# Kernel optimization log

Measured on AMD Instinct MI355X. Metric: run time of the kernel, lower is better.

The kernel has to match this reference:

```python
import jax, jax.numpy as jnp
import numpy as np

B, S, E, H = 4, 1024, 1024, 16
D = E // H  # per-head dim


def setup_inputs() -> dict:
    key = jax.random.key(0)
    ks = jax.random.split(key, 5)
    scale = 1.0 / np.sqrt(E)
    x = jax.random.normal(ks[0], (B, S, E), dtype=jnp.float32)
    Wq = jax.random.normal(ks[1], (H, E, D), dtype=jnp.float32) * scale
    Wk = jax.random.normal(ks[2], (H, E, D), dtype=jnp.float32) * scale
    Wv = jax.random.normal(ks[3], (H, E, D), dtype=jnp.float32) * scale
    W_O = jax.random.normal(ks[4], (E, E), dtype=jnp.float32) * scale
    return {"x": x, "Wq": Wq, "Wk": Wk, "Wv": Wv, "W_O": W_O}


def reference(x, Wq, Wk, Wv, W_O):
    # Batched-over-heads equivalent of the per-head Python loop.
    q = jnp.einsum('bse,hed->bhsd', x, Wq)
    k = jnp.einsum('bse,hed->bhsd', x, Wk)
    v = jnp.einsum('bse,hed->bhsd', x, Wv)
    scores = jnp.einsum('bhqd,bhkd->bhqk', q, k) / jnp.sqrt(jnp.float32(D))
    causal = jnp.tril(jnp.ones((S, S), dtype=bool))  # [S,S]
    scores = jnp.where(causal, scores, jnp.finfo(scores.dtype).min)
    attn = jax.nn.softmax(scores, axis=-1)
    heads = jnp.einsum('bhqk,bhkd->bhqd', attn, v)
    # concat heads along feature dim -> (B, S, E)
    concat = heads.transpose(0, 2, 1, 3).reshape(B, S, E)
    # Faithful to `self.W_O @ concatenated_outputs` (valid since S == E):
    # broadcasts W_O (E,E) against concat's trailing (S,E) matrices.
    output = jnp.matmul(W_O, concat)
    return output
```

## Files before the change

### kernel.cpp

```cpp
#include <hip/hip_runtime.h>
#include <hip/hip_bf16.h>
#include <math.h>

#define B_ 4
#define S_ 1024
#define E_ 1024
#define H_ 16
#define D_ 64

typedef __attribute__((ext_vector_type(8))) short   s16x8;
typedef __attribute__((ext_vector_type(8))) unsigned short u16x8;
typedef __attribute__((ext_vector_type(4))) unsigned short u16x4;
typedef __attribute__((ext_vector_type(4))) float   f32x4;
typedef unsigned short u16;

__device__ __forceinline__ u16 f2bf(float f) {
    union { float f; unsigned u; } v; v.f = f;
    unsigned u = v.u + 0x7FFFu + ((v.u >> 16) & 1u);
    return (u16)(u >> 16);
}
__device__ __forceinline__ float bf2f(u16 h) {
    union { unsigned u; float f; } v; v.u = ((unsigned)h) << 16;
    return v.f;
}
__device__ __forceinline__ void splitf(float f, u16& h, u16& l) {
    h = f2bf(f);
    l = f2bf(f - bf2f(h));
}

#define MFMA(a, b, c) __builtin_amdgcn_mfma_f32_16x16x32_bf16((a), (b), (c), 0, 0, 0)

#define LDR 40

__global__ __launch_bounds__(256) void split_f32(
    const float* __restrict__ src, u16* __restrict__ h, u16* __restrict__ l)
{
    const size_t i = ((size_t)blockIdx.x * 256 + threadIdx.x) * 8;
    f32x4 a = *(const f32x4*)(src + i);
    f32x4 b = *(const f32x4*)(src + i + 4);
    u16x8 hv, lv;
    #pragma unroll
    for (int j = 0; j < 4; j++) {
        u16 hh, ll;
        splitf(a[j], hh, ll); hv[j]     = hh; lv[j]     = ll;
        splitf(b[j], hh, ll); hv[j + 4] = hh; lv[j + 4] = ll;
    }
    *(u16x8*)(h + i) = hv;
    *(u16x8*)(l + i) = lv;
}

__global__ __launch_bounds__(256) void split_wT(
    const float* __restrict__ Wq, const float* __restrict__ Wk, const float* __restrict__ Wv,
    u16* __restrict__ wth, u16* __restrict__ wtl)
{
    __shared__ float T[64][65];
    const int e0 = blockIdx.x * 64;
    const int h  = blockIdx.y;
    const int w  = blockIdx.z;
    const float* W = (w == 0) ? Wq : (w == 1) ? Wk : Wv;

    const int tid = threadIdx.x;
    const int r4  = tid >> 4;
    const int c4  = (tid & 15) * 4;

    #pragma unroll
    for (int p = 0; p < 4; p++) {
        const int r = p * 16 + r4;
        f32x4 v = *(const f32x4*)(W + ((size_t)h * E_ + e0 + r) * D_ + c4);
        #pragma unroll
        for (int j = 0; j < 4; j++) T[r][c4 + j] = v[j];
    }
    __syncthreads();
    #pragma unroll
    for (int p = 0; p < 4; p++) {
        const int d = p * 16 + r4;
        u16x4 oh, ol;
        #pragma unroll
        for (int j = 0; j < 4; j++) {
            u16 hh, ll;
            splitf(T[c4 + j][d], hh, ll);
            oh[j] = hh; ol[j] = ll;
        }
        const size_t n   = (size_t)w * 1024 + h * 64 + d;
        const size_t off = n * E_ + e0 + c4;
        *(u16x4*)(wth + off) = oh;
        *(u16x4*)(wtl + off) = ol;
    }
}

__global__ __launch_bounds__(256) void qkv_gemm(
    const u16* __restrict__ xh, const u16* __restrict__ xl,
    const u16* __restrict__ wth, const u16* __restrict__ wtl,
    u16* __restrict__ qh, u16* __restrict__ ql,
    u16* __restrict__ kh, u16* __restrict__ kl,
    u16* __restrict__ vth, u16* __restrict__ vtl)
{
    __shared__ __align__(16) u16 Ah[128][LDR], Al[128][LDR], Bh[128][LDR], Bl[128][LDR];

    const int tid = threadIdx.x;
    const int m0  = blockIdx.x * 128;
    const int n0  = blockIdx.y * 128;
    const int w   = n0 >> 10;

    const int wid  = tid >> 6, lane = tid & 63;
    const int wr   = wid >> 1, wc = wid & 1;
    const int lrow = lane & 15, lk = lane >> 4;

    const int sr = tid >> 1;
    const int sh = (tid & 1) * 16;

    f32x4 acc[4][4] = {};

    for (int k0 = 0; k0 < E_; k0 += 32) {
        __syncthreads();
        {
            const size_t ao = (size_t)(m0 + sr) * E_ + k0 + sh;
            *(u16x8*)&Ah[sr][sh]     = *(const u16x8*)(xh + ao);
            *(u16x8*)&Ah[sr][sh + 8] = *(const u16x8*)(xh + ao + 8);
            *(u16x8*)&Al[sr][sh]     = *(const u16x8*)(xl + ao);
            *(u16x8*)&Al[sr][sh + 8] = *(const u16x8*)(xl + ao + 8);
            const size_t bo = (size_t)(n0 + sr) * E_ + k0 + sh;
            *(u16x8*)&Bh[sr][sh]     = *(const u16x8*)(wth + bo);
            *(u16x8*)&Bh[sr][sh + 8] = *(const u16x8*)(wth + bo + 8);
            *(u16x8*)&Bl[sr][sh]     = *(const u16x8*)(wtl + bo);
            *(u16x8*)&Bl[sr][sh + 8] = *(const u16x8*)(wtl + bo + 8);
        }
        __syncthreads();

        s16x8 fXh[4], fXl[4], fWh[4], fWl[4];
        #pragma unroll
        for (int i = 0; i < 4; i++) {
            fXh[i] = *(const s16x8*)&Ah[wr * 64 + i * 16 + lrow][lk * 8];
            fXl[i] = *(const s16x8*)&Al[wr * 64 + i * 16 + lrow][lk * 8];
            fWh[i] = *(const s16x8*)&Bh[wc * 64 + i * 16 + lrow][lk * 8];
            fWl[i] = *(const s16x8*)&Bl[wc * 64 + i * 16 + lrow][lk * 8];
        }
        __builtin_amdgcn_s_setprio(1);
        if (w < 2) {
            #pragma unroll
            for (int i = 0; i < 4; i++)
                #pragma unroll
                for (int j = 0; j < 4; j++) {
                    acc[i][j] = MFMA(fWh[i], fXh[j], acc[i][j]);
                    acc[i][j] = MFMA(fWl[i], fXh[j], acc[i][j]);
                    acc[i][j] = MFMA(fWh[i], fXl[j], acc[i][j]);
                }
        } else {
            #pragma unroll
            for (int i = 0; i < 4; i++)
                #pragma unroll
                for (int j = 0; j < 4; j++) {
                    acc[i][j] = MFMA(fXh[i], fWh[j], acc[i][j]);
                    acc[i][j] = MFMA(fXl[i], fWh[j], acc[i][j]);
                    acc[i][j] = MFMA(fXh[i], fWl[j], acc[i][j]);
                }
        }
        __builtin_amdgcn_s_setprio(0);
    }

    const int nloc = n0 & 1023;
    if (w < 2) {
        u16* Yh = (w == 0) ? qh : kh;
        u16* Yl = (w == 0) ? ql : kl;
        const float sc = (w == 0) ? 0.125f : 1.0f;
        #pragma unroll
        for (int i = 0; i < 4; i++) {
            const int nn = nloc + wc * 64 + i * 16 + lk * 4;
            const int hh2 = nn >> 6, d0 = nn & 63;
            #pragma unroll
            for (int j = 0; j < 4; j++) {
                const int mrow = m0 + wr * 64 + j * 16 + lrow;
                const int b = mrow >> 10, s = mrow & 1023;
                u16x4 oh, ol;
                #pragma unroll
                for (int r = 0; r < 4; r++) {
                    u16 hhv, llv;
                    splitf(acc[i][j][r] * sc, hhv, llv);
                    oh[r] = hhv; ol[r] = llv;
                }
                const size_t off = (((size_t)b * H_ + hh2) * S_ + s) * D_ + d0;
                *(u16x4*)(Yh + off) = oh;
                *(u16x4*)(Yl + off) = ol;
            }
        }
    } else {
        #pragma unroll
        for (int i = 0; i < 4; i++) {
            const int mrow = m0 + wr * 64 + i * 16 + lk * 4;
            const int b = mrow >> 10, s = mrow & 1023;
            #pragma unroll
            for (int j = 0; j < 4; j++) {
                const int nn = nloc + wc * 64 + j * 16 + lrow;
                const int hh2 = nn >> 6, d0 = nn & 63;
                u16x4 oh, ol;
                #pragma unroll
                for (int r = 0; r < 4; r++) {
                    u16 hhv, llv;
                    splitf(acc[i][j][r], hhv, llv);
                    oh[r] = hhv; ol[r] = llv;
                }
                const size_t off = (((size_t)b * H_ + hh2) * D_ + d0) * S_ + s;
                *(u16x4*)(vth + off) = oh;
                *(u16x4*)(vtl + off) = ol;
            }
        }
    }
}

__global__ __launch_bounds__(256) void attn(
    const u16* __restrict__ qh, const u16* __restrict__ ql,
    const u16* __restrict__ kh, const u16* __restrict__ kl,
    const u16* __restrict__ vth, const u16* __restrict__ vtl,
    u16* __restrict__ CTh, u16* __restrict__ CTl)
{
    const int qt = 15 - blockIdx.x;
    const int bh = blockIdx.y;

    __shared__ __align__(16) u16 Kh[64][72], Kl[64][72];
    __shared__ __align__(16) u16 Vh[64][72], Vl[64][72];
    __shared__ __align__(16) u16 Ph[4][16][72], Pl[4][16][72];

    const int tid = threadIdx.x, wid = tid >> 6, lane = tid & 63;
    const int lrow = lane & 15, lk = lane >> 4;
    const int q0g = qt * 64 + wid * 16;

    s16x8 fQh[2], fQl[2];
    {
        const size_t qoff = ((size_t)bh * S_ + q0g + lrow) * D_;
        #pragma unroll
        for (int ks = 0; ks < 2; ks++) {
            fQh[ks] = *(const s16x8*)(qh + qoff + ks * 32 + lk * 8);
            fQl[ks] = *(const s16x8*)(ql + qoff + ks * 32 + lk * 8);
        }
    }

    f32x4 accO[4] = {};
    float m_r[4], l_r[4];
    #pragma unroll
    for (int r = 0; r < 4; r++) { m_r[r] = -INFINITY; l_r[r] = 0.0f; }

    const u16* Kbh = kh  + (size_t)bh * S_ * D_;
    const u16* Kbl = kl  + (size_t)bh * S_ * D_;
    const u16* Vbh = vth + (size_t)bh * D_ * S_;
    const u16* Vbl = vtl + (size_t)bh * D_ * S_;

    const int rk = tid >> 2, ck = (tid & 3) * 16;

    u16x8 pf0, pf1, pf2, pf3, pf4, pf5, pf6, pf7;
#define ISSUE(c0_) { \
        const size_t ko = (size_t)((c0_) + rk) * D_ + ck; \
        pf0 = *(const u16x8*)(Kbh + ko);     pf1 = *(const u16x8*)(Kbh + ko + 8); \
        pf2 = *(const u16x8*)(Kbl + ko);     pf3 = *(const u16x8*)(Kbl + ko + 8); \
        const size_t vo = (size_t)rk * S_ + (c0_) + ck; \
        pf4 = *(const u16x8*)(Vbh + vo);     pf5 = *(const u16x8*)(Vbh + vo + 8); \
        pf6 = *(const u16x8*)(Vbl + vo);     pf7 = *(const u16x8*)(Vbl + vo + 8); }

    ISSUE(0)

    for (int t = 0; t <= qt; t++) {
        const int c0 = t * 64;
        __syncthreads();
        *(u16x8*)&Kh[rk][ck]     = pf0;  *(u16x8*)&Kh[rk][ck + 8] = pf1;
        *(u16x8*)&Kl[rk][ck]     = pf2;  *(u16x8*)&Kl[rk][ck + 8] = pf3;
        *(u16x8*)&Vh[rk][ck]     = pf4;  *(u16x8*)&Vh[rk][ck + 8] = pf5;
        *(u16x8*)&Vl[rk][ck]     = pf6;  *(u16x8*)&Vl[rk][ck + 8] = pf7;
        __syncthreads();

        if (t < qt) ISSUE(c0 + 64)

        f32x4 accS[4] = {};
        __builtin_amdgcn_s_setprio(1);
        #pragma unroll
        for (int nf = 0; nf < 4; nf++) {
            #pragma unroll
            for (int ks = 0; ks < 2; ks++) {
                const s16x8 kfh = *(const s16x8*)&Kh[nf * 16 + lrow][ks * 32 + lk * 8];
                const s16x8 kfl = *(const s16x8*)&Kl[nf * 16 + lrow][ks * 32 + lk * 8];
                accS[nf] = MFMA(fQh[ks], kfh, accS[nf]);
                accS[nf] = MFMA(fQl[ks], kfh, accS[nf]);
                accS[nf] = MFMA(fQh[ks], kfl, accS[nf]);
            }
        }
        __builtin_amdgcn_s_setprio(0);

        if (c0 + 63 > q0g) {
            #pragma unroll
            for (int nf = 0; nf < 4; nf++)
                #pragma unroll
                for (int r = 0; r < 4; r++) {
                    if (c0 + nf * 16 + lrow > q0g + lk * 4 + r) accS[nf][r] = -INFINITY;
                }
        }

        float rs[4];
        #pragma unroll
        for (int r = 0; r < 4; r++) {
            float v = fmaxf(fmaxf(accS[0][r], accS[1][r]), fmaxf(accS[2][r], accS[3][r]));
            #pragma unroll
            for (int d_ = 1; d_ < 16; d_ <<= 1) v = fmaxf(v, __shfl_xor(v, d_));
            const float mnew = fmaxf(m_r[r], v);
            rs[r] = __expf(m_r[r] - mnew);
            m_r[r] = mnew;
            float sum = 0.0f;
            #pragma unroll
            for (int nf = 0; nf < 4; nf++) {
                const float p = __expf(accS[nf][r] - mnew);
                accS[nf][r] = p;
                sum += p;
            }
            #pragma unroll
            for (int d_ = 1; d_ < 16; d_ <<= 1) sum += __shfl_xor(sum, d_);
            l_r[r] = l_r[r] * rs[r] + sum;
        }

        #pragma unroll
        for (int nf = 0; nf < 4; nf++)
            #pragma unroll
            for (int r = 0; r < 4; r++) {
                u16 hh, ll;
                splitf(accS[nf][r], hh, ll);
                Ph[wid][lk * 4 + r][nf * 16 + lrow] = hh;
                Pl[wid][lk * 4 + r][nf * 16 + lrow] = ll;
            }
        #pragma unroll
        for (int df = 0; df < 4; df++)
            #pragma unroll
            for (int r = 0; r < 4; r++) accO[df][r] *= rs[r];

        s16x8 fPh[2], fPl[2];
        #pragma unroll
        for (int ks = 0; ks < 2; ks++) {
            fPh[ks] = *(const s16x8*)&Ph[wid][lrow][ks * 32 + lk * 8];
            fPl[ks] = *(const s16x8*)&Pl[wid][lrow][ks * 32 + lk * 8];
        }
        __builtin_amdgcn_s_setprio(1);
        #pragma unroll
        for (int df = 0; df < 4; df++) {
            #pragma unroll
            for (int ks = 0; ks < 2; ks++) {
                const s16x8 vfh = *(const s16x8*)&Vh[df * 16 + lrow][ks * 32 + lk * 8];
                const s16x8 vfl = *(const s16x8*)&Vl[df * 16 + lrow][ks * 32 + lk * 8];
                accO[df] = MFMA(fPh[ks], vfh, accO[df]);
                accO[df] = MFMA(fPl[ks], vfh, accO[df]);
                accO[df] = MFMA(fPh[ks], vfl, accO[df]);
            }
        }
        __builtin_amdgcn_s_setprio(0);
    }
#undef ISSUE

    const int b = bh >> 4, h = bh & 15;
    float inv[4];
    #pragma unroll
    for (int r = 0; r < 4; r++) inv[r] = 1.0f / l_r[r];
    #pragma unroll
    for (int df = 0; df < 4; df++) {
        const int e = h * 64 + df * 16 + lrow;
        const int s = q0g + lk * 4;
        u16x4 oh, ol;
        #pragma unroll
        for (int r = 0; r < 4; r++) {
            u16 hh, ll;
            splitf(accO[df][r] * inv[r], hh, ll);
            oh[r] = hh; ol[r] = ll;
        }
        const size_t off = ((size_t)b * E_ + e) * S_ + s;
        *(u16x4*)(CTh + off) = oh;
        *(u16x4*)(CTl + off) = ol;
    }
}

__global__ __launch_bounds__(256) void out_gemm(
    const u16* __restrict__ CTh, const u16* __restrict__ CTl,
    const u16* __restrict__ woh, const u16* __restrict__ wol,
    float* __restrict__ out)
{
    __shared__ __align__(16) u16 Ah[128][LDR], Al[128][LDR], Bh[128][LDR], Bl[128][LDR];

    const int tid = threadIdx.x;
    const int j0 = blockIdx.x * 128;
    const int i0 = blockIdx.y * 128;
    const int b  = blockIdx.z;

    const int wid = tid >> 6, lane = tid & 63;
    const int wr = wid >> 1, wc = wid & 1;
    const int lrow = lane & 15, lk = lane >> 4;

    const int sr = tid >> 1;
    const int sh = (tid & 1) * 16;

    f32x4 acc[4][4] = {};

    for (int k0 = 0; k0 < S_; k0 += 32) {
        __syncthreads();
        {
            const size_t ao = ((size_t)b * E_ + j0 + sr) * S_ + k0 + sh;
            *(u16x8*)&Ah[sr][sh]     = *(const u16x8*)(CTh + ao);
            *(u16x8*)&Ah[sr][sh + 8] = *(const u16x8*)(CTh + ao + 8);
            *(u16x8*)&Al[sr][sh]     = *(const u16x8*)(CTl + ao);
            *(u16x8*)&Al[sr][sh + 8] = *(const u16x8*)(CTl + ao + 8);
            const size_t bo = (size_t)(i0 + sr) * S_ + k0 + sh;
            *(u16x8*)&Bh[sr][sh]     = *(const u16x8*)(woh + bo);
            *(u16x8*)&Bh[sr][sh + 8] = *(const u16x8*)(woh + bo + 8);
            *(u16x8*)&Bl[sr][sh]     = *(const u16x8*)(wol + bo);
            *(u16x8*)&Bl[sr][sh + 8] = *(const u16x8*)(wol + bo + 8);
        }
        __syncthreads();

        s16x8 fAh[4], fAl[4], fBh[4], fBl[4];
        #pragma unroll
        for (int i = 0; i < 4; i++) {
            fAh[i] = *(const s16x8*)&Ah[wr * 64 + i * 16 + lrow][lk * 8];
            fAl[i] = *(const s16x8*)&Al[wr * 64 + i * 16 + lrow][lk * 8];
            fBh[i] = *(const s16x8*)&Bh[wc * 64 + i * 16 + lrow][lk * 8];
            fBl[i] = *(const s16x8*)&Bl[wc * 64 + i * 16 + lrow][lk * 8];
        }
        __builtin_amdgcn_s_setprio(1);
        #pragma unroll
        for (int i = 0; i < 4; i++)
            #pragma unroll
            for (int j = 0; j < 4; j++) {
                acc[i][j] = MFMA(fAh[i], fBh[j], acc[i][j]);
                acc[i][j] = MFMA(fAl[i], fBh[j], acc[i][j]);
                acc[i][j] = MFMA(fAh[i], fBl[j], acc[i][j]);
            }
        __builtin_amdgcn_s_setprio(0);
    }

    #pragma unroll
    for (int i = 0; i < 4; i++) {
        const int jj = j0 + wr * 64 + i * 16 + lk * 4;
        #pragma unroll
        for (int j = 0; j < 4; j++) {
            const int ii = i0 + wc * 64 + j * 16 + lrow;
            float* dst = out + ((size_t)b * E_ + ii) * E_ + jj;
            *(f32x4*)dst = acc[i][j];
        }
    }
}

extern "C" void kernel_launch(void* const* d_in, const int* in_sizes, int n_in,
                              void* d_out, int out_size, void* d_ws, size_t ws_size,
                              hipStream_t stream)
{
    const float* x   = (const float*)d_in[0];
    const float* Wq  = (const float*)d_in[1];
    const float* Wk  = (const float*)d_in[2];
    const float* Wv  = (const float*)d_in[3];
    const float* W_O = (const float*)d_in[4];
    float* out = (float*)d_out;

    const size_t N = (size_t)B_ * S_ * E_;
    u16* p = (u16*)d_ws;
    u16* qh  = p;            u16* ql  = p + 1 * N;
    u16* kh  = p + 2 * N;    u16* kl  = p + 3 * N;
    u16* vth = p + 4 * N;    u16* vtl = p + 5 * N;
    u16* xh  = p + 6 * N;    u16* xl  = p + 7 * N;
    u16* wth = p + 8 * N;
    u16* wtl = wth + (size_t)3 * E_ * E_;
    u16* CTh = xh;           u16* CTl = xl;
    u16* woh = wth;          u16* wol = wtl;

    split_f32<<<2048, 256, 0, stream>>>(x, xh, xl);
    split_wT<<<dim3(16, 16, 3), 256, 0, stream>>>(Wq, Wk, Wv, wth, wtl);
    qkv_gemm<<<dim3(32, 24), 256, 0, stream>>>(xh, xl, wth, wtl, qh, ql, kh, kl, vth, vtl);
    split_f32<<<512, 256, 0, stream>>>(W_O, woh, wol);
    attn<<<dim3(16, 64), 256, 0, stream>>>(qh, ql, kh, kl, vth, vtl, CTh, CTl);
    out_gemm<<<dim3(8, 8, 4), 256, 0, stream>>>(CTh, CTl, woh, wol, out);
}
```

Measured before the change: 349.0 us.

## Pre-tile GEMM operands into contiguous 128x32 blocks and load via global_load_lds

The split kernels now write x, the QKV weights, W_O and the attention output in a block-tiled layout where each 128x32 K-slice is contiguous. The QKV and output GEMMs can then fill LDS with direct global-to-LDS 16-byte loads, one wave per operand, instead of loading into registers and storing to LDS. LDS rows lose their padding (stride 32 instead of 40), so fragment reads may hit bank conflicts. W_O's low half now sits at a different workspace offset.

```diff
diff --git a/kernel.cpp b/kernel.cpp
--- a/kernel.cpp
+++ b/kernel.cpp
@@ -30,12 +30,20 @@
 
 #define MFMA(a, b, c) __builtin_amdgcn_mfma_f32_16x16x32_bf16((a), (b), (c), 0, 0, 0)
 
-#define LDR 40
-
-__global__ __launch_bounds__(256) void split_f32(
-    const float* __restrict__ src, u16* __restrict__ h, u16* __restrict__ l)
+__device__ __forceinline__ void gload16(const u16* g, u16* l) {
+    __builtin_amdgcn_global_load_lds(
+        (const __attribute__((address_space(1))) void*)g,
+        (__attribute__((address_space(3))) void*)l, 16, 0, 0);
+}
+
+#define TILE_E   4096
+#define BLK_E    131072
+
+__global__ __launch_bounds__(256) void tile_rows(
+    const float* __restrict__ src, u16* __restrict__ th, u16* __restrict__ tl)
 {
     const size_t i = ((size_t)blockIdx.x * 256 + threadIdx.x) * 8;
+    const int m = (int)(i >> 10), e = (int)(i & 1023);
     f32x4 a = *(const f32x4*)(src + i);
     f32x4 b = *(const f32x4*)(src + i + 4);
     u16x8 hv, lv;
@@ -45,11 +53,13 @@
         splitf(a[j], hh, ll); hv[j]     = hh; lv[j]     = ll;
         splitf(b[j], hh, ll); hv[j + 4] = hh; lv[j + 4] = ll;
     }
-    *(u16x8*)(h + i) = hv;
-    *(u16x8*)(l + i) = lv;
-}
-
-__global__ __launch_bounds__(256) void split_wT(
+    const int mblk = m >> 7, row = m & 127, ks = e >> 5, col = e & 31;
+    const size_t off = ((size_t)(mblk * 32 + ks) * 128 + row) * 32 + col;
+    *(u16x8*)(th + off) = hv;
+    *(u16x8*)(tl + off) = lv;
+}
+
+__global__ __launch_bounds__(256) void tile_w(
     const float* __restrict__ Wq, const float* __restrict__ Wk, const float* __restrict__ Wv,
     u16* __restrict__ wth, u16* __restrict__ wtl)
 {
@@ -71,6 +81,9 @@
         for (int j = 0; j < 4; j++) T[r][c4 + j] = v[j];
     }
     __syncthreads();
+    const int nblk = w * 8 + (h >> 1);
+    const int ks   = (e0 + c4) >> 5;
+    const int col  = (e0 + c4) & 31;
     #pragma unroll
     for (int p = 0; p < 4; p++) {
         const int d = p * 16 + r4;
@@ -81,49 +94,49 @@
             splitf(T[c4 + j][d], hh, ll);
             oh[j] = hh; ol[j] = ll;
         }
-        const size_t n   = (size_t)w * 1024 + h * 64 + d;
-        const size_t off = n * E_ + e0 + c4;
+        const int row = (h & 1) * 64 + d;
+        const size_t off = ((size_t)(nblk * 32 + ks) * 128 + row) * 32 + col;
         *(u16x4*)(wth + off) = oh;
         *(u16x4*)(wtl + off) = ol;
     }
 }
 
 __global__ __launch_bounds__(256) void qkv_gemm(
-    const u16* __restrict__ xh, const u16* __restrict__ xl,
+    const u16* __restrict__ xsh, const u16* __restrict__ xsl,
     const u16* __restrict__ wth, const u16* __restrict__ wtl,
     u16* __restrict__ qh, u16* __restrict__ ql,
     u16* __restrict__ kh, u16* __restrict__ kl,
     u16* __restrict__ vth, u16* __restrict__ vtl)
 {
-    __shared__ __align__(16) u16 Ah[128][LDR], Al[128][LDR], Bh[128][LDR], Bl[128][LDR];
-
-    const int tid = threadIdx.x;
-    const int m0  = blockIdx.x * 128;
-    const int n0  = blockIdx.y * 128;
-    const int w   = n0 >> 10;
+    __shared__ __align__(16) u16 Ah[128][32], Al[128][32], Bh[128][32], Bl[128][32];
+
+    const int tid  = threadIdx.x;
+    const int mblk = blockIdx.x;
+    const int nblk = blockIdx.y;
+    const int n0   = nblk * 128;
+    const int w    = n0 >> 10;
 
     const int wid  = tid >> 6, lane = tid & 63;
     const int wr   = wid >> 1, wc = wid & 1;
     const int lrow = lane & 15, lk = lane >> 4;
 
-    const int sr = tid >> 1;
-    const int sh = (tid & 1) * 16;
+    const u16* gsrc;
+    u16* lbase;
+    if      (wid == 0) { gsrc = xsh + (size_t)mblk * BLK_E; lbase = &Ah[0][0]; }
+    else if (wid == 1) { gsrc = xsl + (size_t)mblk * BLK_E; lbase = &Al[0][0]; }
+    else if (wid == 2) { gsrc = wth + (size_t)nblk * BLK_E; lbase = &Bh[0][0]; }
+    else               { gsrc = wtl + (size_t)nblk * BLK_E; lbase = &Bl[0][0]; }
 
     f32x4 acc[4][4] = {};
 
-    for (int k0 = 0; k0 < E_; k0 += 32) {
+    for (int ks = 0; ks < 32; ks++) {
         __syncthreads();
         {
-            const size_t ao = (size_t)(m0 + sr) * E_ + k0 + sh;
-            *(u16x8*)&Ah[sr][sh]     = *(const u16x8*)(xh + ao);
-            *(u16x8*)&Ah[sr][sh + 8] = *(const u16x8*)(xh + ao + 8);
-            *(u16x8*)&Al[sr][sh]     = *(const u16x8*)(xl + ao);
-            *(u16x8*)&Al[sr][sh + 8] = *(const u16x8*)(xl + ao + 8);
-            const size_t bo = (size_t)(n0 + sr) * E_ + k0 + sh;
-            *(u16x8*)&Bh[sr][sh]     = *(const u16x8*)(wth + bo);
-            *(u16x8*)&Bh[sr][sh + 8] = *(const u16x8*)(wth + bo + 8);
-            *(u16x8*)&Bl[sr][sh]     = *(const u16x8*)(wtl + bo);
-            *(u16x8*)&Bl[sr][sh + 8] = *(const u16x8*)(wtl + bo + 8);
+            const u16* s = gsrc + (size_t)ks * TILE_E + lane * 8;
+            u16* l = lbase + lane * 8;
+            #pragma unroll
+            for (int c = 0; c < 8; c++)
+                gload16(s + c * 512, l + c * 512);
         }
         __syncthreads();
 
@@ -158,6 +171,7 @@
         __builtin_amdgcn_s_setprio(0);
     }
 
+    const int m0   = mblk * 128;
     const int nloc = n0 & 1023;
     if (w < 2) {
         u16* Yh = (w == 0) ? qh : kh;
@@ -353,10 +367,12 @@
     float inv[4];
     #pragma unroll
     for (int r = 0; r < 4; r++) inv[r] = 1.0f / l_r[r];
+    const int s0 = q0g + lk * 4;
+    const int kst = s0 >> 5, col = s0 & 31;
     #pragma unroll
     for (int df = 0; df < 4; df++) {
         const int e = h * 64 + df * 16 + lrow;
-        const int s = q0g + lk * 4;
+        const int jblk = e >> 7, row = e & 127;
         u16x4 oh, ol;
         #pragma unroll
         for (int r = 0; r < 4; r++) {
@@ -364,7 +380,8 @@
             splitf(accO[df][r] * inv[r], hh, ll);
             oh[r] = hh; ol[r] = ll;
         }
-        const size_t off = ((size_t)b * E_ + e) * S_ + s;
+        const size_t off = (size_t)b * 1048576 +
+                           ((size_t)(jblk * 32 + kst) * 128 + row) * 32 + col;
         *(u16x4*)(CTh + off) = oh;
         *(u16x4*)(CTl + off) = ol;
     }
@@ -375,35 +392,34 @@
     const u16* __restrict__ woh, const u16* __restrict__ wol,
     float* __restrict__ out)
 {
-    __shared__ __align__(16) u16 Ah[128][LDR], Al[128][LDR], Bh[128][LDR], Bl[128][LDR];
-
-    const int tid = threadIdx.x;
-    const int j0 = blockIdx.x * 128;
-    const int i0 = blockIdx.y * 128;
-    const int b  = blockIdx.z;
+    __shared__ __align__(16) u16 Ah[128][32], Al[128][32], Bh[128][32], Bl[128][32];
+
+    const int tid  = threadIdx.x;
+    const int jblk = blockIdx.x;
+    const int iblk = blockIdx.y;
+    const int b    = blockIdx.z;
 
     const int wid = tid >> 6, lane = tid & 63;
     const int wr = wid >> 1, wc = wid & 1;
     const int lrow = lane & 15, lk = lane >> 4;
 
-    const int sr = tid >> 1;
-    const int sh = (tid & 1) * 16;
+    const u16* gsrc;
+    u16* lbase;
+    if      (wid == 0) { gsrc = CTh + (size_t)b * 1048576 + (size_t)jblk * BLK_E; lbase = &Ah[0][0]; }
+    else if (wid == 1) { gsrc = CTl + (size_t)b * 1048576 + (size_t)jblk * BLK_E; lbase = &Al[0][0]; }
+    else if (wid == 2) { gsrc = woh + (size_t)iblk * BLK_E; lbase = &Bh[0][0]; }
+    else               { gsrc = wol + (size_t)iblk * BLK_E; lbase = &Bl[0][0]; }
 
     f32x4 acc[4][4] = {};
 
-    for (int k0 = 0; k0 < S_; k0 += 32) {
+    for (int ks = 0; ks < 32; ks++) {
         __syncthreads();
         {
-            const size_t ao = ((size_t)b * E_ + j0 + sr) * S_ + k0 + sh;
-            *(u16x8*)&Ah[sr][sh]     = *(const u16x8*)(CTh + ao);
-            *(u16x8*)&Ah[sr][sh + 8] = *(const u16x8*)(CTh + ao + 8);
-            *(u16x8*)&Al[sr][sh]     = *(const u16x8*)(CTl + ao);
-            *(u16x8*)&Al[sr][sh + 8] = *(const u16x8*)(CTl + ao + 8);
-            const size_t bo = (size_t)(i0 + sr) * S_ + k0 + sh;
-            *(u16x8*)&Bh[sr][sh]     = *(const u16x8*)(woh + bo);
-            *(u16x8*)&Bh[sr][sh + 8] = *(const u16x8*)(woh + bo + 8);
-            *(u16x8*)&Bl[sr][sh]     = *(const u16x8*)(wol + bo);
-            *(u16x8*)&Bl[sr][sh + 8] = *(const u16x8*)(wol + bo + 8);
+            const u16* s = gsrc + (size_t)ks * TILE_E + lane * 8;
+            u16* l = lbase + lane * 8;
+            #pragma unroll
+            for (int c = 0; c < 8; c++)
+                gload16(s + c * 512, l + c * 512);
         }
         __syncthreads();
 
@@ -427,6 +443,7 @@
         __builtin_amdgcn_s_setprio(0);
     }
 
+    const int j0 = jblk * 128, i0 = iblk * 128;
     #pragma unroll
     for (int i = 0; i < 4; i++) {
         const int jj = j0 + wr * 64 + i * 16 + lk * 4;
@@ -455,16 +472,17 @@
     u16* qh  = p;            u16* ql  = p + 1 * N;
     u16* kh  = p + 2 * N;    u16* kl  = p + 3 * N;
     u16* vth = p + 4 * N;    u16* vtl = p + 5 * N;
-    u16* xh  = p + 6 * N;    u16* xl  = p + 7 * N;
+    u16* xsh = p + 6 * N;    u16* xsl = p + 7 * N;
     u16* wth = p + 8 * N;
     u16* wtl = wth + (size_t)3 * E_ * E_;
-    u16* CTh = xh;           u16* CTl = xl;
-    u16* woh = wth;          u16* wol = wtl;
-
-    split_f32<<<2048, 256, 0, stream>>>(x, xh, xl);
-    split_wT<<<dim3(16, 16, 3), 256, 0, stream>>>(Wq, Wk, Wv, wth, wtl);
-    qkv_gemm<<<dim3(32, 24), 256, 0, stream>>>(xh, xl, wth, wtl, qh, ql, kh, kl, vth, vtl);
-    split_f32<<<512, 256, 0, stream>>>(W_O, woh, wol);
+    u16* CTh = xsh;          u16* CTl = xsl;
+    u16* woh = wth;          u16* wol = wth + (size_t)E_ * E_;
+
+    tile_rows<<<2048, 256, 0, stream>>>(x, xsh, xsl);
+    tile_w<<<dim3(16, 16, 3), 256, 0, stream>>>(Wq, Wk, Wv, wth, wtl);
+    qkv_gemm<<<dim3(32, 24), 256, 0, stream>>>(xsh, xsl, wth, wtl,
+                                               qh, ql, kh, kl, vth, vtl);
+    tile_rows<<<512, 256, 0, stream>>>(W_O, woh, wol);
     attn<<<dim3(16, 64), 256, 0, stream>>>(qh, ql, kh, kl, vth, vtl, CTh, CTl);
     out_gemm<<<dim3(8, 8, 4), 256, 0, stream>>>(CTh, CTl, woh, wol, out);
 }
```

After: 329.3 us. 1.06x faster.
